# Performance work log

Measured on AMD Instinct MI355X. Metric: run time of the kernel, lower is better.

The kernel has to match this reference:

```python
import jax, jax.numpy as jnp
import numpy as np

V, T, E, H, L, B = 50257, 1024, 1024, 16, 12, 4
HD = E // H
FF = 4 * E
EPS = 1e-5


def layer_norm(x, g, b):
    m = jnp.mean(x, axis=-1, keepdims=True)
    v = jnp.mean((x - m) ** 2, axis=-1, keepdims=True)
    return (x - m) * jax.lax.rsqrt(v + EPS) * g + b


def setup_inputs() -> dict:
    key = jax.random.key(0)
    ks = jax.random.split(key, 24)
    s = 0.02
    inp = {
        'idx': jax.random.randint(ks[0], (B, T), 0, V),
        'targets': jax.random.randint(ks[1], (B, T), 0, V),
        'tok_emb': jax.random.normal(ks[2], (V, E), jnp.float32) * s,
        'pos_emb': jax.random.normal(ks[3], (T, E), jnp.float32) * s,
        'Wq': jax.random.normal(ks[4], (L, E, H, HD), jnp.float32) * s,
        'Wk': jax.random.normal(ks[5], (L, E, H, HD), jnp.float32) * s,
        'Wv': jax.random.normal(ks[6], (L, E, H, HD), jnp.float32) * s,
        'Wo': jax.random.normal(ks[7], (L, E, E), jnp.float32) * s,
        'bo': jnp.zeros((L, E), jnp.float32),
        'ln1_g': jnp.ones((L, E), jnp.float32),
        'ln1_b': jnp.zeros((L, E), jnp.float32),
        'ln2_g': jnp.ones((L, E), jnp.float32),
        'ln2_b': jnp.zeros((L, E), jnp.float32),
        'W1': jax.random.normal(ks[8], (L, E, FF), jnp.float32) * s,
        'b1': jnp.zeros((L, FF), jnp.float32),
        'W2': jax.random.normal(ks[9], (L, FF, E), jnp.float32) * s,
        'b2': jnp.zeros((L, E), jnp.float32),
        'lnf_g': jnp.ones((E,), jnp.float32),
        'lnf_b': jnp.zeros((E,), jnp.float32),
        'Whead': jax.random.normal(ks[10], (E, V), jnp.float32) * s,
        'bhead': jnp.zeros((V,), jnp.float32),
    }
    return inp


def forward(idx, targets, tok_emb, pos_emb, Wq, Wk, Wv, Wo, bo, ln1_g, ln1_b,
            ln2_g, ln2_b, W1, b1, W2, b2, lnf_g, lnf_b, Whead, bhead):
    Bc, Tc = idx.shape
    x = tok_emb[idx] + pos_emb[:Tc]  # [B,T,E]
    scale = HD ** -0.5
    causal = jnp.tril(jnp.ones((Tc, Tc), bool))
    for l in range(L):
        h = layer_norm(x, ln1_g[l], ln1_b[l])
        q = jnp.einsum('bte,ehd->bthd', h, Wq[l])
        k = jnp.einsum('bte,ehd->bthd', h, Wk[l])
        v = jnp.einsum('bte,ehd->bthd', h, Wv[l])
        wei = jnp.einsum('bqhd,bkhd->bhqk', q, k) * scale
        wei = jnp.where(causal, wei, -jnp.inf)
        wei = jax.nn.softmax(wei, axis=-1)
        att = jnp.einsum('bhqk,bkhd->bqhd', wei, v).reshape(Bc, Tc, E)
        x = x + att @ Wo[l] + bo[l]
        h = layer_norm(x, ln2_g[l], ln2_b[l])
        # torch nn.GELU default is exact (erf) gelu
        ff = jax.nn.gelu(h @ W1[l] + b1[l], approximate=False) @ W2[l] + b2[l]
        x = x + ff
    x = layer_norm(x, lnf_g, lnf_b)
    logits = x @ Whead + bhead  # [B,T,V]
    logp = jax.nn.log_softmax(logits, axis=-1)
    nll = -jnp.take_along_axis(logp, targets[..., None], axis=-1)[..., 0]
    loss = jnp.mean(nll)
    return logits, loss


def reference(idx, targets, tok_emb, pos_emb, Wq, Wk, Wv, Wo, bo, ln1_g, ln1_b,
              ln2_g, ln2_b, W1, b1, W2, b2, lnf_g, lnf_b, Whead, bhead):
    return forward(idx, targets, tok_emb, pos_emb, Wq, Wk, Wv, Wo, bo, ln1_g,
                   ln1_b, ln2_g, ln2_b, W1, b1, W2, b2, lnf_g, lnf_b, Whead, bhead)
```

## Files before the change

kernel.cpp:

```cpp
#include <hip/hip_runtime.h>
#include <cstdint>
#include <cstddef>

typedef unsigned short u16;
typedef __bf16 bf16x8 __attribute__((ext_vector_type(8)));
typedef float f32x4 __attribute__((ext_vector_type(4)));
typedef unsigned short u16x8 __attribute__((ext_vector_type(8)));
typedef unsigned short u16x4 __attribute__((ext_vector_type(4)));

constexpr int cV  = 50257;
constexpr int cVp = 50432;
constexpr int cNT = cVp / 256;
constexpr int cT  = 1024;
constexpr int cE  = 1024;
constexpr int cL  = 12;
constexpr int cFF = 4096;
constexpr int cBT = 4096;

__device__ __forceinline__ u16 f2bf(float f) {
  union { float f; unsigned u; } x; x.f = f;
  unsigned r = x.u + 0x7fffu + ((x.u >> 16) & 1u);
  return (u16)(r >> 16);
}

__device__ __forceinline__ void gload16(const void* g, void* l) {
  __builtin_amdgcn_global_load_lds(
      (const __attribute__((address_space(1))) void*)g,
      (__attribute__((address_space(3))) void*)l, 16, 0, 0);
}

__device__ __forceinline__ int swzoff(int row, int chunk) {
  return ((chunk ^ (row & 7) ^ ((row >> 3) & 7)) << 4);
}

__device__ __forceinline__ int xcd_swz(int id, int nwg) {
  if ((nwg & 7) == 0) { const int q = nwg >> 3; return (id & 7) * q + (id >> 3); }
  return id;
}

__global__ __launch_bounds__(256) void k_embed(const int* __restrict__ idx,
    const float* __restrict__ tok, const float* __restrict__ pos,
    float* __restrict__ x) {
  const int row = blockIdx.x;
  const int t = row & (cT - 1);
  const int tk = idx[row];
  const float4* tv = (const float4*)(tok + (size_t)tk * cE);
  const float4* pv = (const float4*)(pos + (size_t)t * cE);
  float4* xv = (float4*)(x + (size_t)row * cE);
  const int i = threadIdx.x;
  float4 a = tv[i];
  float4 p = pv[i];
  a.x += p.x; a.y += p.y; a.z += p.z; a.w += p.w;
  xv[i] = a;
}

__global__ __launch_bounds__(256) void k_ln(const float* __restrict__ x,
    const float* __restrict__ gw, const float* __restrict__ bw,
    u16* __restrict__ out) {
  const int row = blockIdx.x;
  const int t = threadIdx.x;
  const float4 v = ((const float4*)(x + (size_t)row * cE))[t];
  float s1 = v.x + v.y + v.z + v.w;
  float s2 = v.x * v.x + v.y * v.y + v.z * v.z + v.w * v.w;
  #pragma unroll
  for (int off = 32; off; off >>= 1) {
    s1 += __shfl_xor(s1, off);
    s2 += __shfl_xor(s2, off);
  }
  __shared__ float red[8];
  const int wid = t >> 6;
  if ((t & 63) == 0) { red[wid] = s1; red[4 + wid] = s2; }
  __syncthreads();
  s1 = red[0] + red[1] + red[2] + red[3];
  s2 = red[4] + red[5] + red[6] + red[7];
  const float mean = s1 * (1.0f / cE);
  const float var = s2 * (1.0f / cE) - mean * mean;
  const float rs = rsqrtf(var + 1e-5f);
  const float4 g4 = ((const float4*)gw)[t];
  const float4 b4 = ((const float4*)bw)[t];
  u16x4 o;
  o[0] = f2bf((v.x - mean) * rs * g4.x + b4.x);
  o[1] = f2bf((v.y - mean) * rs * g4.y + b4.y);
  o[2] = f2bf((v.z - mean) * rs * g4.z + b4.z);
  o[3] = f2bf((v.w - mean) * rs * g4.w + b4.w);
  *(u16x4*)(out + (size_t)row * cE + t * 4) = o;
}

__global__ __launch_bounds__(256) void k_cvt_t(const float* __restrict__ src,
    u16* __restrict__ dst, int K, int Nsrc, size_t sstride, size_t dstride) {
  __shared__ float tile[32][33];
  const float* s = src + blockIdx.z * sstride;
  u16* d = dst + blockIdx.z * dstride;
  const int n0 = blockIdx.x * 32, k0 = blockIdx.y * 32;
  const int t = threadIdx.x;
  const int c = t & 31, r0 = t >> 5;
  #pragma unroll
  for (int i = 0; i < 4; ++i) {
    const int kl = r0 + i * 8;
    const int n = n0 + c;
    tile[kl][c] = (n < Nsrc) ? s[(size_t)(k0 + kl) * Nsrc + n] : 0.0f;
  }
  __syncthreads();
  #pragma unroll
  for (int i = 0; i < 4; ++i) {
    const int nl = r0 + i * 8;
    d[(size_t)(n0 + nl) * K + k0 + c] = f2bf(tile[c][nl]);
  }
}

__device__ __forceinline__ void stage_half(const u16* __restrict__ Mb, int K,
    int kt, char* lds, int half, int tid) {
  #pragma unroll
  for (int p = 0; p < 2; ++p) {
    const int L = half * 1024 + p * 512 + tid;
    const int row = L >> 3, cc = L & 7;
    gload16(Mb + (size_t)row * K + kt + ((cc ^ (row & 7)) << 3),
            lds + (size_t)L * 16);
  }
}

template<int EPI>
__global__ __launch_bounds__(512) void k_gemm2(
    const u16* __restrict__ A, const u16* __restrict__ Bt,
    const float* __restrict__ bias, u16* __restrict__ obf,
    float* __restrict__ of, int K, int Nout, int ntile, int mt,
    float* __restrict__ pm, float* __restrict__ ps) {
  __shared__ __align__(16) char smem[131072];
  const int tid = threadIdx.x;
  const int lane = tid & 63;
  const int wid = tid >> 6;
  const int wg = xcd_swz((int)blockIdx.x, (int)gridDim.x);
  const int bm = wg % mt;
  const int bn = wg / mt;
  const int wm = wid >> 2, wn = wid & 3;
  const int l15 = lane & 15, lg = lane >> 4;

  f32x4 acc[8][4];
  #pragma unroll
  for (int i = 0; i < 8; ++i)
    #pragma unroll
    for (int j = 0; j < 4; ++j) { f32x4 z = {0.f,0.f,0.f,0.f}; acc[i][j] = z; }

  const u16* Ab = A + (size_t)(bm * 256) * K;
  const u16* Bb = Bt + (size_t)(bn * 256) * K;
  const int nt = K >> 6;

  {
    char* s0 = smem;
    char* s1 = smem + 65536;
    stage_half(Ab, K, 0, s0, 0, tid);
    stage_half(Bb, K, 0, s0 + 32768, 0, tid);
    stage_half(Bb, K, 0, s0 + 32768, 1, tid);
    stage_half(Ab, K, 0, s0, 1, tid);
    const int k1 = (nt > 1) ? 64 : 0;
    stage_half(Ab, K, k1, s1, 0, tid);
    stage_half(Bb, K, k1, s1 + 32768, 0, tid);
    stage_half(Bb, K, k1, s1 + 32768, 1, tid);
  }

  bf16x8 af[4][2], bfr[4][2];
  for (int t = 0; t < nt; ++t) {
    char* cs = smem + ((t & 1) << 16);
    char* co = smem + (((t & 1) ^ 1) << 16);
    const char* csB = cs + 32768;
    const int kn1 = (t + 1 < nt ? t + 1 : nt - 1) << 6;
    const int kn2 = (t + 2 < nt ? t + 2 : nt - 1) << 6;

    asm volatile("s_waitcnt vmcnt(6)" ::: "memory");
    __builtin_amdgcn_s_barrier();

    #pragma unroll
    for (int mi = 0; mi < 4; ++mi) {
      const int row = wm * 128 + mi * 16 + l15;
      #pragma unroll
      for (int kk = 0; kk < 2; ++kk)
        af[mi][kk] = *(const bf16x8*)(cs + row * 128 + (((kk * 4 + lg) ^ (row & 7)) << 4));
    }
    #pragma unroll
    for (int ni = 0; ni < 2; ++ni) {
      const int rowB = wn * 64 + ni * 16 + l15;
      #pragma unroll
      for (int kk = 0; kk < 2; ++kk)
        bfr[ni][kk] = *(const bf16x8*)(csB + rowB * 128 + (((kk * 4 + lg) ^ (rowB & 7)) << 4));
    }
    stage_half(Ab, K, kn1, co, 1, tid);
    __builtin_amdgcn_sched_barrier(0);
    __builtin_amdgcn_s_setprio(1);
    #pragma unroll
    for (int kk = 0; kk < 2; ++kk)
      #pragma unroll
      for (int ni = 0; ni < 2; ++ni)
        #pragma unroll
        for (int mi = 0; mi < 4; ++mi)
          acc[mi][ni] = __builtin_amdgcn_mfma_f32_16x16x32_bf16(af[mi][kk], bfr[ni][kk], acc[mi][ni], 0, 0, 0);
    __builtin_amdgcn_s_setprio(0);
    __builtin_amdgcn_sched_barrier(0);
    __builtin_amdgcn_s_barrier();

    #pragma unroll
    for (int ni = 2; ni < 4; ++ni) {
      const int rowB = wn * 64 + ni * 16 + l15;
      #pragma unroll
      for (int kk = 0; kk < 2; ++kk)
        bfr[ni][kk] = *(const bf16x8*)(csB + rowB * 128 + (((kk * 4 + lg) ^ (rowB & 7)) << 4));
    }
    __builtin_amdgcn_sched_barrier(0);
    __builtin_amdgcn_s_setprio(1);
    #pragma unroll
    for (int kk = 0; kk < 2; ++kk)
      #pragma unroll
      for (int ni = 2; ni < 4; ++ni)
        #pragma unroll
        for (int mi = 0; mi < 4; ++mi)
          acc[mi][ni] = __builtin_amdgcn_mfma_f32_16x16x32_bf16(af[mi][kk], bfr[ni][kk], acc[mi][ni], 0, 0, 0);
    __builtin_amdgcn_s_setprio(0);
    __builtin_amdgcn_sched_barrier(0);
    __builtin_amdgcn_s_barrier();

    #pragma unroll
    for (int mi = 0; mi < 4; ++mi) {
      const int row = wm * 128 + 64 + mi * 16 + l15;
      #pragma unroll
      for (int kk = 0; kk < 2; ++kk)
        af[mi][kk] = *(const bf16x8*)(cs + row * 128 + (((kk * 4 + lg) ^ (row & 7)) << 4));
    }
    stage_half(Ab, K, kn2, cs, 0, tid);
    stage_half(Bb, K, kn2, cs + 32768, 0, tid);
    stage_half(Bb, K, kn2, cs + 32768, 1, tid);
    __builtin_amdgcn_sched_barrier(0);
    __builtin_amdgcn_s_setprio(1);
    #pragma unroll
    for (int kk = 0; kk < 2; ++kk)
      #pragma unroll
      for (int ni = 0; ni < 2; ++ni)
        #pragma unroll
        for (int mi = 0; mi < 4; ++mi)
          acc[4 + mi][ni] = __builtin_amdgcn_mfma_f32_16x16x32_bf16(af[mi][kk], bfr[ni][kk], acc[4 + mi][ni], 0, 0, 0);
    __builtin_amdgcn_s_setprio(0);
    __builtin_amdgcn_sched_barrier(0);
    __builtin_amdgcn_s_barrier();

    __builtin_amdgcn_s_setprio(1);
    #pragma unroll
    for (int kk = 0; kk < 2; ++kk)
      #pragma unroll
      for (int ni = 2; ni < 4; ++ni)
        #pragma unroll
        for (int mi = 0; mi < 4; ++mi)
          acc[4 + mi][ni] = __builtin_amdgcn_mfma_f32_16x16x32_bf16(af[mi][kk], bfr[ni][kk], acc[4 + mi][ni], 0, 0, 0);
    __builtin_amdgcn_s_setprio(0);
    __builtin_amdgcn_sched_barrier(0);
  }
  asm volatile("s_waitcnt vmcnt(0)" ::: "memory");

  if constexpr (EPI == 3) {
    __syncthreads();
    float* pb = (float*)smem;
    #pragma unroll
    for (int m8 = 0; m8 < 8; ++m8) {
      const int grow = bm * 256 + wm * 128 + m8 * 16 + lg * 4;
      float rm[4];
      #pragma unroll
      for (int r = 0; r < 4; ++r) rm[r] = -1e30f;
      #pragma unroll
      for (int ni = 0; ni < 4; ++ni) {
        const int gcol = bn * 256 + wn * 64 + ni * 16 + l15;
        const bool ok = gcol < Nout;
        const float bb = ok ? bias[gcol] : 0.0f;
        #pragma unroll
        for (int r = 0; r < 4; ++r) {
          const float v = ok ? (acc[m8][ni][r] + bb) : -1e30f;
          acc[m8][ni][r] = v;
          if (ok) of[(size_t)(grow + r) * Nout + gcol] = v;
          rm[r] = fmaxf(rm[r], v);
        }
      }
      #pragma unroll
      for (int r = 0; r < 4; ++r) {
        float m = rm[r];
        #pragma unroll
        for (int off = 1; off < 16; off <<= 1) m = fmaxf(m, __shfl_xor(m, off));
        float s = 0.f;
        #pragma unroll
        for (int ni = 0; ni < 4; ++ni) s += __expf(acc[m8][ni][r] - m);
        #pragma unroll
        for (int off = 1; off < 16; off <<= 1) s += __shfl_xor(s, off);
        if (l15 == 0) {
          const int lrow = wm * 128 + m8 * 16 + lg * 4 + r;
          pb[(lrow * 4 + wn) * 2] = m;
          pb[(lrow * 4 + wn) * 2 + 1] = s;
        }
      }
    }
    __syncthreads();
    if (tid < 256) {
      float m = -1e30f, s = 0.f;
      #pragma unroll
      for (int q = 0; q < 4; ++q) {
        const float m2 = pb[(tid * 4 + q) * 2];
        const float s2 = pb[(tid * 4 + q) * 2 + 1];
        const float M = fmaxf(m, m2);
        s = s * __expf(m - M) + s2 * __expf(m2 - M);
        m = M;
      }
      const size_t grow = (size_t)(bm * 256 + tid);
      pm[grow * ntile + bn] = m;
      ps[grow * ntile + bn] = s;
    }
  } else {
    #pragma unroll
    for (int m8 = 0; m8 < 8; ++m8) {
      const int grow = bm * 256 + wm * 128 + m8 * 16 + lg * 4;
      #pragma unroll
      for (int ni = 0; ni < 4; ++ni) {
        const int gcol = bn * 256 + wn * 64 + ni * 16 + l15;
        #pragma unroll
        for (int r = 0; r < 4; ++r) {
          const float a = acc[m8][ni][r];
          if constexpr (EPI == 0) {
            obf[(size_t)(gcol >> 10) * 4194304 + (size_t)(grow + r) * 1024 + (gcol & 1023)] = f2bf(a);
          } else {
            const float gv = a + bias[gcol];
            obf[(size_t)(grow + r) * Nout + gcol] = f2bf(0.5f * gv * (1.0f + erff(gv * 0.70710678118f)));
          }
        }
      }
    }
  }
}

__global__ __launch_bounds__(256) void k_gemm_s(
    const u16* __restrict__ A, const u16* __restrict__ Bt,
    const float* __restrict__ bias, float* __restrict__ of,
    int K, int Nout, int mt) {
  __shared__ __align__(16) char smem[49152];
  const int tid = threadIdx.x;
  const int lane = tid & 63;
  const int wid = tid >> 6;
  const int wg = xcd_swz((int)blockIdx.x, (int)gridDim.x);
  const int bm = wg % mt;
  const int bn = wg / mt;
  const int wr = wid >> 1, wc = wid & 1;
  const int l15 = lane & 15, lg = lane >> 4;

  f32x4 acc[2][4];
  #pragma unroll
  for (int i = 0; i < 2; ++i)
    #pragma unroll
    for (int j = 0; j < 4; ++j) { f32x4 z = {0.f,0.f,0.f,0.f}; acc[i][j] = z; }

  const u16* Ab = A + (size_t)(bm * 64) * K;
  const u16* Bb = Bt + (size_t)(bn * 128) * K;
  const int nt = K >> 6;

  auto stage = [&](int t, char* buf) {
    const int kt = (t < nt ? t : nt - 1) << 6;
    #pragma unroll
    for (int p = 0; p < 2; ++p) {
      const int L = p * 256 + tid;
      const int row = L >> 3, cc = L & 7;
      gload16(Ab + (size_t)row * K + kt + ((cc ^ (row & 7)) << 3), buf + L * 16);
    }
    #pragma unroll
    for (int p = 0; p < 4; ++p) {
      const int L = p * 256 + tid;
      const int row = L >> 3, cc = L & 7;
      gload16(Bb + (size_t)row * K + kt + ((cc ^ (row & 7)) << 3), buf + 8192 + L * 16);
    }
  };
  stage(0, smem);
  stage(1, smem + 24576);

  for (int t = 0; t < nt; ++t) {
    char* cs = smem + ((t & 1) ? 24576 : 0);
    const char* csB = cs + 8192;
    asm volatile("s_waitcnt vmcnt(6)" ::: "memory");
    __builtin_amdgcn_s_barrier();

    bf16x8 af[2][2], bfr[4][2];
    #pragma unroll
    for (int mi = 0; mi < 2; ++mi) {
      const int row = wr * 32 + mi * 16 + l15;
      #pragma unroll
      for (int kk = 0; kk < 2; ++kk)
        af[mi][kk] = *(const bf16x8*)(cs + row * 128 + (((kk * 4 + lg) ^ (row & 7)) << 4));
    }
    #pragma unroll
    for (int ni = 0; ni < 4; ++ni) {
      const int row = wc * 64 + ni * 16 + l15;
      #pragma unroll
      for (int kk = 0; kk < 2; ++kk)
        bfr[ni][kk] = *(const bf16x8*)(csB + row * 128 + (((kk * 4 + lg) ^ (row & 7)) << 4));
    }
    __builtin_amdgcn_sched_barrier(0);
    __builtin_amdgcn_s_setprio(1);
    #pragma unroll
    for (int ni = 0; ni < 4; ++ni)
      #pragma unroll
      for (int mi = 0; mi < 2; ++mi)
        acc[mi][ni] = __builtin_amdgcn_mfma_f32_16x16x32_bf16(af[mi][0], bfr[ni][0], acc[mi][ni], 0, 0, 0);
    __builtin_amdgcn_s_setprio(0);
    __builtin_amdgcn_sched_barrier(0);
    asm volatile("s_waitcnt lgkmcnt(0)" ::: "memory");
    __builtin_amdgcn_sched_barrier(0);
    __builtin_amdgcn_s_barrier();

    stage(t + 2, cs);
    __builtin_amdgcn_sched_barrier(0);
    __builtin_amdgcn_s_setprio(1);
    #pragma unroll
    for (int ni = 0; ni < 4; ++ni)
      #pragma unroll
      for (int mi = 0; mi < 2; ++mi)
        acc[mi][ni] = __builtin_amdgcn_mfma_f32_16x16x32_bf16(af[mi][1], bfr[ni][1], acc[mi][ni], 0, 0, 0);
    __builtin_amdgcn_s_setprio(0);
    __builtin_amdgcn_sched_barrier(0);
  }
  asm volatile("s_waitcnt vmcnt(0)" ::: "memory");

  #pragma unroll
  for (int mi = 0; mi < 2; ++mi) {
    const int grow = bm * 64 + wr * 32 + mi * 16 + lg * 4;
    #pragma unroll
    for (int ni = 0; ni < 4; ++ni) {
      const int gcol = bn * 128 + wc * 64 + ni * 16 + l15;
      #pragma unroll
      for (int r = 0; r < 4; ++r)
        of[(size_t)(grow + r) * Nout + gcol] += acc[mi][ni][r] + bias[gcol];
    }
  }
}

__global__ __launch_bounds__(256) void k_gemm_legacy3(
    const u16* __restrict__ A, const float* __restrict__ B0,
    const float* __restrict__ bias, float* __restrict__ of,
    int M, int N, int K) {
  __shared__ u16 Al[128 * 32];
  __shared__ u16 Bl[32 * 128];
  const int tid = threadIdx.x;
  const int lane = tid & 63;
  const int wid = tid >> 6;
  const int bn = blockIdx.x;
  const int bm = blockIdx.y;
  const int wr = wid >> 1, wc = wid & 1;
  const int l15 = lane & 15, lg = lane >> 4;
  f32x4 acc[4][4];
  #pragma unroll
  for (int i = 0; i < 4; ++i)
    #pragma unroll
    for (int j = 0; j < 4; ++j) { f32x4 z = {0.f,0.f,0.f,0.f}; acc[i][j] = z; }
  const u16* Abase = A + (size_t)(bm * 128) * K;
  const int ar0 = tid >> 2;
  const int ac0 = (tid & 3) * 8;
  const int brow = tid >> 3;
  const int bc0 = (tid & 7) * 16;
  for (int kt = 0; kt < K; kt += 32) {
    *(u16x8*)(Al + ar0 * 32 + ac0) =
        *(const u16x8*)(Abase + (size_t)ar0 * K + kt + ac0);
    *(u16x8*)(Al + (ar0 + 64) * 32 + ac0) =
        *(const u16x8*)(Abase + (size_t)(ar0 + 64) * K + kt + ac0);
    {
      const float* bsrc = B0 + (size_t)(kt + brow) * N + bn * 128 + bc0;
      alignas(16) u16 tmp[16];
      const int colbase = bn * 128 + bc0;
      #pragma unroll
      for (int q = 0; q < 16; ++q)
        tmp[q] = f2bf((colbase + q < N) ? bsrc[q] : 0.0f);
      *(u16x8*)(Bl + brow * 128 + bc0) = *(const u16x8*)tmp;
      *(u16x8*)(Bl + brow * 128 + bc0 + 8) = *(const u16x8*)(tmp + 8);
    }
    __syncthreads();
    bf16x8 af[4];
    #pragma unroll
    for (int mi = 0; mi < 4; ++mi)
      af[mi] = *(const bf16x8*)(Al + (wr * 64 + mi * 16 + l15) * 32 + lg * 8);
    #pragma unroll
    for (int ni = 0; ni < 4; ++ni) {
      u16x8 tv;
      #pragma unroll
      for (int i = 0; i < 8; ++i)
        tv[i] = Bl[(lg * 8 + i) * 128 + wc * 64 + ni * 16 + l15];
      const bf16x8 bfr = __builtin_bit_cast(bf16x8, tv);
      #pragma unroll
      for (int mi = 0; mi < 4; ++mi)
        acc[mi][ni] = __builtin_amdgcn_mfma_f32_16x16x32_bf16(af[mi], bfr, acc[mi][ni], 0, 0, 0);
    }
    __syncthreads();
  }
  #pragma unroll
  for (int mi = 0; mi < 4; ++mi) {
    const int grow = bm * 128 + wr * 64 + mi * 16 + lg * 4;
    #pragma unroll
    for (int ni = 0; ni < 4; ++ni) {
      const int gcol = bn * 128 + wc * 64 + ni * 16 + l15;
      #pragma unroll
      for (int r = 0; r < 4; ++r)
        if (gcol < N) of[(size_t)(grow + r) * N + gcol] = acc[mi][ni][r] + bias[gcol];
    }
  }
}

__global__ __launch_bounds__(256, 2) void k_attn(
    const u16* __restrict__ qg, const u16* __restrict__ kg,
    const u16* __restrict__ vg, u16* __restrict__ og) {
  __shared__ u16 Kl[64 * 64];
  __shared__ u16 Vt[64 * 64];
  __shared__ u16 Pl[4][16 * 64];
  const int tid = threadIdx.x;
  const int lane = tid & 63;
  const int w = tid >> 6;
  const int qt = blockIdx.x;
  const int bh = blockIdx.y;
  const int b = bh >> 4, h = bh & 15;
  const int l15 = lane & 15, lg = lane >> 4;
  char* KlB = (char*)Kl;
  char* VtB = (char*)Vt;
  char* PlB = (char*)(Pl[w]);

  const size_t qrow0 = (size_t)b * cT + qt * 64 + w * 16;
  bf16x8 aq[2];
  #pragma unroll
  for (int c = 0; c < 2; ++c)
    aq[c] = *(const bf16x8*)(qg + (qrow0 + l15) * cE + h * 64 + c * 32 + lg * 8);

  f32x4 acco[4];
  #pragma unroll
  for (int j = 0; j < 4; ++j) { f32x4 z = {0.f,0.f,0.f,0.f}; acco[j] = z; }
  float mrun[4], lrun[4];
  #pragma unroll
  for (int r = 0; r < 4; ++r) { mrun[r] = -1e30f; lrun[r] = 0.f; }

  for (int kt = 0; kt <= qt; ++kt) {
    const size_t krow0 = (size_t)b * cT + kt * 64;
    #pragma unroll
    for (int u = 0; u < 2; ++u) {
      const int un = tid + u * 256;
      const int rr = un >> 3, c8 = (un & 7) * 8;
      *(u16x8*)(KlB + rr * 128 + swzoff(rr, c8 >> 3)) =
          *(const u16x8*)(kg + (krow0 + rr) * cE + h * 64 + c8);
      const u16x8 vv = *(const u16x8*)(vg + (krow0 + rr) * cE + h * 64 + c8);
      #pragma unroll
      for (int i = 0; i < 8; ++i)
        *(u16*)(VtB + (c8 + i) * 128 + swzoff(c8 + i, rr >> 3) + (rr & 7) * 2) = vv[i];
    }
    __syncthreads();

    f32x4 s[4];
    #pragma unroll
    for (int j = 0; j < 4; ++j) { f32x4 z = {0.f,0.f,0.f,0.f}; s[j] = z; }
    #pragma unroll
    for (int c = 0; c < 2; ++c) {
      #pragma unroll
      for (int j = 0; j < 4; ++j) {
        const int n = j * 16 + l15;
        const bf16x8 kb2 = *(const bf16x8*)(KlB + n * 128 + swzoff(n, c * 4 + lg));
        s[j] = __builtin_amdgcn_mfma_f32_16x16x32_bf16(aq[c], kb2, s[j], 0, 0, 0);
      }
    }

    float sv[4][4];
    const bool diag = (kt == qt);
    #pragma unroll
    for (int j = 0; j < 4; ++j)
      #pragma unroll
      for (int r = 0; r < 4; ++r) {
        float xs = s[j][r] * 0.125f;
        if (diag && (j * 16 + l15) > (w * 16 + lg * 4 + r)) xs = -1e30f;
        sv[j][r] = xs;
      }

    float corr[4];
    #pragma unroll
    for (int r = 0; r < 4; ++r) {
      float mx = fmaxf(fmaxf(sv[0][r], sv[1][r]), fmaxf(sv[2][r], sv[3][r]));
      #pragma unroll
      for (int off = 1; off < 16; off <<= 1) mx = fmaxf(mx, __shfl_xor(mx, off));
      const float mnew = fmaxf(mrun[r], mx);
      corr[r] = __expf(mrun[r] - mnew);
      float rs = 0.f;
      #pragma unroll
      for (int j = 0; j < 4; ++j) {
        const float p = __expf(sv[j][r] - mnew);
        sv[j][r] = p;
        rs += p;
      }
      #pragma unroll
      for (int off = 1; off < 16; off <<= 1) rs += __shfl_xor(rs, off);
      lrun[r] = lrun[r] * corr[r] + rs;
      mrun[r] = mnew;
    }

    #pragma unroll
    for (int j = 0; j < 4; ++j)
      #pragma unroll
      for (int r = 0; r < 4; ++r) {
        const int qr = lg * 4 + r, kc = j * 16 + l15;
        *(u16*)(PlB + qr * 128 + swzoff(qr, kc >> 3) + (kc & 7) * 2) = f2bf(sv[j][r]);
        acco[j][r] *= corr[r];
      }

    #pragma unroll
    for (int c = 0; c < 2; ++c) {
      const bf16x8 pa = *(const bf16x8*)(PlB + l15 * 128 + swzoff(l15, c * 4 + lg));
      #pragma unroll
      for (int j = 0; j < 4; ++j) {
        const int n = j * 16 + l15;
        const bf16x8 vb2 = *(const bf16x8*)(VtB + n * 128 + swzoff(n, c * 4 + lg));
        acco[j] = __builtin_amdgcn_mfma_f32_16x16x32_bf16(pa, vb2, acco[j], 0, 0, 0);
      }
    }
    __syncthreads();
  }

  #pragma unroll
  for (int j = 0; j < 4; ++j)
    #pragma unroll
    for (int r = 0; r < 4; ++r)
      og[(qrow0 + lg * 4 + r) * cE + h * 64 + j * 16 + l15] = f2bf(acco[j][r] / lrun[r]);
}

__global__ __launch_bounds__(256) void k_nll2(const float* __restrict__ pm,
    const float* __restrict__ ps, const float* __restrict__ logits,
    const int* __restrict__ tgt, float* __restrict__ nll, int NT) {
  const int row = blockIdx.x * 4 + (threadIdx.x >> 6);
  const int lane = threadIdx.x & 63;
  float m = -1e30f, s = 0.f;
  for (int i = lane; i < NT; i += 64) {
    const float m2 = pm[(size_t)row * NT + i];
    const float s2 = ps[(size_t)row * NT + i];
    const float M = fmaxf(m, m2);
    s = s * __expf(m - M) + s2 * __expf(m2 - M);
    m = M;
  }
  #pragma unroll
  for (int off = 1; off < 64; off <<= 1) {
    const float m2 = __shfl_xor(m, off);
    const float s2 = __shfl_xor(s, off);
    const float M = fmaxf(m, m2);
    s = s * __expf(m - M) + s2 * __expf(m2 - M);
    m = M;
  }
  if (lane == 0)
    nll[row] = logf(s) + m - logits[(size_t)row * cV + tgt[row]];
}

__global__ __launch_bounds__(256) void k_nll(const float* __restrict__ logits,
    const int* __restrict__ tgt, float* __restrict__ nll) {
  const int row = blockIdx.x;
  const float* lp = logits + (size_t)row * cV;
  const int t = threadIdx.x;
  __shared__ float red[8];
  const int wid = t >> 6, lane = t & 63;
  float mx = -1e30f;
  for (int i = t; i < cV; i += 256) mx = fmaxf(mx, lp[i]);
  #pragma unroll
  for (int off = 32; off; off >>= 1) mx = fmaxf(mx, __shfl_xor(mx, off));
  if (lane == 0) red[wid] = mx;
  __syncthreads();
  mx = fmaxf(fmaxf(red[0], red[1]), fmaxf(red[2], red[3]));
  float s = 0.f;
  for (int i = t; i < cV; i += 256) s += __expf(lp[i] - mx);
  #pragma unroll
  for (int off = 32; off; off >>= 1) s += __shfl_xor(s, off);
  if (lane == 0) red[4 + wid] = s;
  __syncthreads();
  if (t == 0) {
    s = red[4] + red[5] + red[6] + red[7];
    nll[row] = logf(s) + mx - lp[tgt[row]];
  }
}

__global__ __launch_bounds__(256) void k_loss(const float* __restrict__ nll,
    float* __restrict__ out) {
  const int t = threadIdx.x;
  float s = 0.f;
  for (int i = t; i < cBT; i += 256) s += nll[i];
  #pragma unroll
  for (int off = 32; off; off >>= 1) s += __shfl_xor(s, off);
  __shared__ float red[4];
  if ((t & 63) == 0) red[t >> 6] = s;
  __syncthreads();
  if (t == 0) out[0] = (red[0] + red[1] + red[2] + red[3]) * (1.0f / cBT);
}

extern "C" void kernel_launch(void* const* d_in, const int* in_sizes, int n_in,
                              void* d_out, int out_size, void* d_ws, size_t ws_size,
                              hipStream_t stream) {
  const int*   idx  = (const int*)d_in[0];
  const int*   tgt  = (const int*)d_in[1];
  const float* tok  = (const float*)d_in[2];
  const float* pos  = (const float*)d_in[3];
  const float* Wq   = (const float*)d_in[4];
  const float* Wk   = (const float*)d_in[5];
  const float* Wv   = (const float*)d_in[6];
  const float* Wo   = (const float*)d_in[7];
  const float* bo   = (const float*)d_in[8];
  const float* ln1g = (const float*)d_in[9];
  const float* ln1b = (const float*)d_in[10];
  const float* ln2g = (const float*)d_in[11];
  const float* ln2b = (const float*)d_in[12];
  const float* W1   = (const float*)d_in[13];
  const float* b1   = (const float*)d_in[14];
  const float* W2   = (const float*)d_in[15];
  const float* b2   = (const float*)d_in[16];
  const float* lnfg = (const float*)d_in[17];
  const float* lnfb = (const float*)d_in[18];
  const float* Wh   = (const float*)d_in[19];
  const float* bh   = (const float*)d_in[20];

  char* ob = (char*)d_out;
  float* x    = (float*)ob;
  u16* hb     = (u16*)(ob + (16u << 20));
  u16* qb     = (u16*)(ob + (24u << 20));
  u16* kb     = (u16*)(ob + (32u << 20));
  u16* vb     = (u16*)(ob + (40u << 20));
  u16* abuf   = (u16*)(ob + (48u << 20));
  u16* fbuf   = (u16*)(ob + (56u << 20));
  u16* W3T    = (u16*)(ob + (128u << 20));
  u16* WoT    = (u16*)(ob + (200u << 20));
  u16* W1T    = (u16*)(ob + (224u << 20));
  u16* W2T    = (u16*)(ob + (320u << 20));
  u16* hf     = (u16*)d_ws;
  float* nll  = (float*)((char*)d_ws + 8388608);
  u16* WheadT = (u16*)((char*)d_ws + 8404992);
  const size_t whead_end = 8404992u + (size_t)cVp * cE * 2u;
  float* pmax = (float*)((char*)d_ws + whead_end);
  float* psum = (float*)((char*)d_ws + whead_end + (size_t)cBT * cNT * 4);
  const size_t ws_need = whead_end + 2u * (size_t)cBT * cNT * 4;
  const bool fast_head = ws_size >= ws_need;

  float* logits = (float*)d_out;
  float* loss = logits + (size_t)cBT * cV;

  const dim3 blk(256);
  const size_t e2 = (size_t)cE * cE, ef = (size_t)cE * cFF;

  k_cvt_t<<<dim3(32, 32, cL), blk, 0, stream>>>(Wq, W3T,          cE, cE, e2, 3 * e2);
  k_cvt_t<<<dim3(32, 32, cL), blk, 0, stream>>>(Wk, W3T + e2,     cE, cE, e2, 3 * e2);
  k_cvt_t<<<dim3(32, 32, cL), blk, 0, stream>>>(Wv, W3T + 2 * e2, cE, cE, e2, 3 * e2);
  k_cvt_t<<<dim3(32, 32, cL), blk, 0, stream>>>(Wo, WoT, cE, cE, e2, e2);
  k_cvt_t<<<dim3(128, 32, cL), blk, 0, stream>>>(W1, W1T, cE, cFF, ef, ef);
  k_cvt_t<<<dim3(32, 128, cL), blk, 0, stream>>>(W2, W2T, cFF, cE, ef, ef);
  if (fast_head)
    k_cvt_t<<<dim3(cVp / 32, 32, 1), blk, 0, stream>>>(Wh, WheadT, cE, cV, 0, 0);

  k_embed<<<dim3(cBT), blk, 0, stream>>>(idx, tok, pos, x);
  for (int l = 0; l < cL; ++l) {
    k_ln<<<dim3(cBT), blk, 0, stream>>>(x, ln1g + l * cE, ln1b + l * cE, hb);
    k_gemm2<0><<<dim3(192), dim3(512), 0, stream>>>(hb, W3T + l * 3 * e2,
        nullptr, qb, nullptr, cE, 3072, 0, 16, nullptr, nullptr);
    k_attn<<<dim3(16, 64), blk, 0, stream>>>(qb, kb, vb, abuf);
    k_gemm_s<<<dim3(512), blk, 0, stream>>>(abuf, WoT + l * e2, bo + l * cE, x, cE, cE, 64);
    k_ln<<<dim3(cBT), blk, 0, stream>>>(x, ln2g + l * cE, ln2b + l * cE, hb);
    k_gemm2<2><<<dim3(256), dim3(512), 0, stream>>>(hb, W1T + l * ef,
        b1 + l * cFF, fbuf, nullptr, cE, cFF, 0, 16, nullptr, nullptr);
    k_gemm_s<<<dim3(512), blk, 0, stream>>>(fbuf, W2T + l * ef, b2 + l * cE, x, cFF, cE, 64);
  }
  k_ln<<<dim3(cBT), blk, 0, stream>>>(x, lnfg, lnfb, hf);
  if (fast_head) {
    k_gemm2<3><<<dim3(16 * cNT), dim3(512), 0, stream>>>(hf, WheadT, bh,
        nullptr, logits, cE, cV, cNT, 16, pmax, psum);
    k_nll2<<<dim3(cBT / 4), blk, 0, stream>>>(pmax, psum, logits, tgt, nll, cNT);
  } else {
    k_gemm_legacy3<<<dim3(393, 32), blk, 0, stream>>>(hf, Wh, bh, logits, cBT, cV, cE);
    k_nll<<<dim3(cBT), blk, 0, stream>>>(logits, tgt, nll);
  }
  k_loss<<<dim3(1), blk, 0, stream>>>(nll, loss);
}
```

Measured before the change: 4.663 ms.

## Shrink k_gemm2 tile to 128x256 with K=32 double buffer

Replaces the 256x256, K=64 triple-staged GEMM pipeline with a simpler 128x256 tile using K=32 steps and a plain two-buffer LDS scheme (48KB instead of 128KB), launch bounds set to allow more resident blocks, and XCD swizzle removed. Grids double so the small QKV/FF1 GEMMs fill more CUs. The cost is lower arithmetic intensity per tile, a full vmcnt(0) wait plus a barrier every iteration, and loss of the XCD-aware block ordering for L2 locality.

```diff
diff --git a/kernel.cpp b/kernel.cpp
--- a/kernel.cpp
+++ b/kernel.cpp
@@ -108,157 +108,87 @@
   }
 }
 
-__device__ __forceinline__ void stage_half(const u16* __restrict__ Mb, int K,
-    int kt, char* lds, int half, int tid) {
-  #pragma unroll
-  for (int p = 0; p < 2; ++p) {
-    const int L = half * 1024 + p * 512 + tid;
-    const int row = L >> 3, cc = L & 7;
-    gload16(Mb + (size_t)row * K + kt + ((cc ^ (row & 7)) << 3),
-            lds + (size_t)L * 16);
-  }
-}
-
 template<int EPI>
-__global__ __launch_bounds__(512) void k_gemm2(
+__global__ __launch_bounds__(512, 4) void k_gemm2(
     const u16* __restrict__ A, const u16* __restrict__ Bt,
     const float* __restrict__ bias, u16* __restrict__ obf,
     float* __restrict__ of, int K, int Nout, int ntile, int mt,
     float* __restrict__ pm, float* __restrict__ ps) {
-  __shared__ __align__(16) char smem[131072];
+  __shared__ __align__(16) char smem[49152];
   const int tid = threadIdx.x;
   const int lane = tid & 63;
   const int wid = tid >> 6;
-  const int wg = xcd_swz((int)blockIdx.x, (int)gridDim.x);
+  const int wg = (int)blockIdx.x;
   const int bm = wg % mt;
   const int bn = wg / mt;
   const int wm = wid >> 2, wn = wid & 3;
   const int l15 = lane & 15, lg = lane >> 4;
 
-  f32x4 acc[8][4];
-  #pragma unroll
-  for (int i = 0; i < 8; ++i)
+  f32x4 acc[4][4];
+  #pragma unroll
+  for (int i = 0; i < 4; ++i)
     #pragma unroll
     for (int j = 0; j < 4; ++j) { f32x4 z = {0.f,0.f,0.f,0.f}; acc[i][j] = z; }
 
-  const u16* Ab = A + (size_t)(bm * 256) * K;
+  const u16* Ab = A + (size_t)(bm * 128) * K;
   const u16* Bb = Bt + (size_t)(bn * 256) * K;
-  const int nt = K >> 6;
-
-  {
-    char* s0 = smem;
-    char* s1 = smem + 65536;
-    stage_half(Ab, K, 0, s0, 0, tid);
-    stage_half(Bb, K, 0, s0 + 32768, 0, tid);
-    stage_half(Bb, K, 0, s0 + 32768, 1, tid);
-    stage_half(Ab, K, 0, s0, 1, tid);
-    const int k1 = (nt > 1) ? 64 : 0;
-    stage_half(Ab, K, k1, s1, 0, tid);
-    stage_half(Bb, K, k1, s1 + 32768, 0, tid);
-    stage_half(Bb, K, k1, s1 + 32768, 1, tid);
-  }
-
-  bf16x8 af[4][2], bfr[4][2];
+  const int nt = K >> 5;
+
+  auto stage = [&](int t) {
+    char* buf = smem + ((t & 1) ? 24576 : 0);
+    const int kt = t << 5;
+    {
+      const int r = tid >> 2, c = tid & 3;
+      gload16(Ab + (size_t)r * K + kt + ((c ^ ((r >> 1) & 3)) << 3),
+              buf + tid * 16);
+    }
+    #pragma unroll
+    for (int p = 0; p < 2; ++p) {
+      const int L = p * 512 + tid;
+      const int r = L >> 2, c = L & 3;
+      gload16(Bb + (size_t)r * K + kt + ((c ^ ((r >> 1) & 3)) << 3),
+              buf + 8192 + L * 16);
+    }
+  };
+
+  stage(0);
+  asm volatile("s_waitcnt vmcnt(0)" ::: "memory");
+  __builtin_amdgcn_s_barrier();
+
   for (int t = 0; t < nt; ++t) {
-    char* cs = smem + ((t & 1) << 16);
-    char* co = smem + (((t & 1) ^ 1) << 16);
-    const char* csB = cs + 32768;
-    const int kn1 = (t + 1 < nt ? t + 1 : nt - 1) << 6;
-    const int kn2 = (t + 2 < nt ? t + 2 : nt - 1) << 6;
-
-    asm volatile("s_waitcnt vmcnt(6)" ::: "memory");
-    __builtin_amdgcn_s_barrier();
-
+    if (t + 1 < nt) stage(t + 1);
+    char* cs = smem + ((t & 1) ? 24576 : 0);
+    const char* csB = cs + 8192;
+    bf16x8 af[4], bfr[4];
     #pragma unroll
     for (int mi = 0; mi < 4; ++mi) {
-      const int row = wm * 128 + mi * 16 + l15;
-      #pragma unroll
-      for (int kk = 0; kk < 2; ++kk)
-        af[mi][kk] = *(const bf16x8*)(cs + row * 128 + (((kk * 4 + lg) ^ (row & 7)) << 4));
-    }
-    #pragma unroll
-    for (int ni = 0; ni < 2; ++ni) {
-      const int rowB = wn * 64 + ni * 16 + l15;
-      #pragma unroll
-      for (int kk = 0; kk < 2; ++kk)
-        bfr[ni][kk] = *(const bf16x8*)(csB + rowB * 128 + (((kk * 4 + lg) ^ (rowB & 7)) << 4));
-    }
-    stage_half(Ab, K, kn1, co, 1, tid);
+      const int row = wm * 64 + mi * 16 + l15;
+      af[mi] = *(const bf16x8*)(cs + row * 64 + ((lg ^ ((row >> 1) & 3)) << 4));
+    }
+    #pragma unroll
+    for (int ni = 0; ni < 4; ++ni) {
+      const int row = wn * 64 + ni * 16 + l15;
+      bfr[ni] = *(const bf16x8*)(csB + row * 64 + ((lg ^ ((row >> 1) & 3)) << 4));
+    }
     __builtin_amdgcn_sched_barrier(0);
     __builtin_amdgcn_s_setprio(1);
     #pragma unroll
-    for (int kk = 0; kk < 2; ++kk)
-      #pragma unroll
-      for (int ni = 0; ni < 2; ++ni)
-        #pragma unroll
-        for (int mi = 0; mi < 4; ++mi)
-          acc[mi][ni] = __builtin_amdgcn_mfma_f32_16x16x32_bf16(af[mi][kk], bfr[ni][kk], acc[mi][ni], 0, 0, 0);
+    for (int ni = 0; ni < 4; ++ni)
+      #pragma unroll
+      for (int mi = 0; mi < 4; ++mi)
+        acc[mi][ni] = __builtin_amdgcn_mfma_f32_16x16x32_bf16(af[mi], bfr[ni], acc[mi][ni], 0, 0, 0);
     __builtin_amdgcn_s_setprio(0);
     __builtin_amdgcn_sched_barrier(0);
+    asm volatile("s_waitcnt vmcnt(0)" ::: "memory");
     __builtin_amdgcn_s_barrier();
-
-    #pragma unroll
-    for (int ni = 2; ni < 4; ++ni) {
-      const int rowB = wn * 64 + ni * 16 + l15;
-      #pragma unroll
-      for (int kk = 0; kk < 2; ++kk)
-        bfr[ni][kk] = *(const bf16x8*)(csB + rowB * 128 + (((kk * 4 + lg) ^ (rowB & 7)) << 4));
-    }
-    __builtin_amdgcn_sched_barrier(0);
-    __builtin_amdgcn_s_setprio(1);
-    #pragma unroll
-    for (int kk = 0; kk < 2; ++kk)
-      #pragma unroll
-      for (int ni = 2; ni < 4; ++ni)
-        #pragma unroll
-        for (int mi = 0; mi < 4; ++mi)
-          acc[mi][ni] = __builtin_amdgcn_mfma_f32_16x16x32_bf16(af[mi][kk], bfr[ni][kk], acc[mi][ni], 0, 0, 0);
-    __builtin_amdgcn_s_setprio(0);
-    __builtin_amdgcn_sched_barrier(0);
-    __builtin_amdgcn_s_barrier();
-
-    #pragma unroll
-    for (int mi = 0; mi < 4; ++mi) {
-      const int row = wm * 128 + 64 + mi * 16 + l15;
-      #pragma unroll
-      for (int kk = 0; kk < 2; ++kk)
-        af[mi][kk] = *(const bf16x8*)(cs + row * 128 + (((kk * 4 + lg) ^ (row & 7)) << 4));
-    }
-    stage_half(Ab, K, kn2, cs, 0, tid);
-    stage_half(Bb, K, kn2, cs + 32768, 0, tid);
-    stage_half(Bb, K, kn2, cs + 32768, 1, tid);
-    __builtin_amdgcn_sched_barrier(0);
-    __builtin_amdgcn_s_setprio(1);
-    #pragma unroll
-    for (int kk = 0; kk < 2; ++kk)
-      #pragma unroll
-      for (int ni = 0; ni < 2; ++ni)
-        #pragma unroll
-        for (int mi = 0; mi < 4; ++mi)
-          acc[4 + mi][ni] = __builtin_amdgcn_mfma_f32_16x16x32_bf16(af[mi][kk], bfr[ni][kk], acc[4 + mi][ni], 0, 0, 0);
-    __builtin_amdgcn_s_setprio(0);
-    __builtin_amdgcn_sched_barrier(0);
-    __builtin_amdgcn_s_barrier();
-
-    __builtin_amdgcn_s_setprio(1);
-    #pragma unroll
-    for (int kk = 0; kk < 2; ++kk)
-      #pragma unroll
-      for (int ni = 2; ni < 4; ++ni)
-        #pragma unroll
-        for (int mi = 0; mi < 4; ++mi)
-          acc[4 + mi][ni] = __builtin_amdgcn_mfma_f32_16x16x32_bf16(af[mi][kk], bfr[ni][kk], acc[4 + mi][ni], 0, 0, 0);
-    __builtin_amdgcn_s_setprio(0);
-    __builtin_amdgcn_sched_barrier(0);
-  }
-  asm volatile("s_waitcnt vmcnt(0)" ::: "memory");
+  }
 
   if constexpr (EPI == 3) {
     __syncthreads();
     float* pb = (float*)smem;
     #pragma unroll
-    for (int m8 = 0; m8 < 8; ++m8) {
-      const int grow = bm * 256 + wm * 128 + m8 * 16 + lg * 4;
+    for (int mi = 0; mi < 4; ++mi) {
+      const int grow = bm * 128 + wm * 64 + mi * 16 + lg * 4;
       float rm[4];
       #pragma unroll
       for (int r = 0; r < 4; ++r) rm[r] = -1e30f;
@@ -269,8 +199,8 @@
         const float bb = ok ? bias[gcol] : 0.0f;
         #pragma unroll
         for (int r = 0; r < 4; ++r) {
-          const float v = ok ? (acc[m8][ni][r] + bb) : -1e30f;
-          acc[m8][ni][r] = v;
+          const float v = ok ? (acc[mi][ni][r] + bb) : -1e30f;
+          acc[mi][ni][r] = v;
           if (ok) of[(size_t)(grow + r) * Nout + gcol] = v;
           rm[r] = fmaxf(rm[r], v);
         }
@@ -282,18 +212,18 @@
         for (int off = 1; off < 16; off <<= 1) m = fmaxf(m, __shfl_xor(m, off));
         float s = 0.f;
         #pragma unroll
-        for (int ni = 0; ni < 4; ++ni) s += __expf(acc[m8][ni][r] - m);
+        for (int ni = 0; ni < 4; ++ni) s += __expf(acc[mi][ni][r] - m);
         #pragma unroll
         for (int off = 1; off < 16; off <<= 1) s += __shfl_xor(s, off);
         if (l15 == 0) {
-          const int lrow = wm * 128 + m8 * 16 + lg * 4 + r;
+          const int lrow = wm * 64 + mi * 16 + lg * 4 + r;
           pb[(lrow * 4 + wn) * 2] = m;
           pb[(lrow * 4 + wn) * 2 + 1] = s;
         }
       }
     }
     __syncthreads();
-    if (tid < 256) {
+    if (tid < 128) {
       float m = -1e30f, s = 0.f;
       #pragma unroll
       for (int q = 0; q < 4; ++q) {
@@ -303,20 +233,20 @@
         s = s * __expf(m - M) + s2 * __expf(m2 - M);
         m = M;
       }
-      const size_t grow = (size_t)(bm * 256 + tid);
+      const size_t grow = (size_t)(bm * 128 + tid);
       pm[grow * ntile + bn] = m;
       ps[grow * ntile + bn] = s;
     }
   } else {
     #pragma unroll
-    for (int m8 = 0; m8 < 8; ++m8) {
-      const int grow = bm * 256 + wm * 128 + m8 * 16 + lg * 4;
+    for (int mi = 0; mi < 4; ++mi) {
+      const int grow = bm * 128 + wm * 64 + mi * 16 + lg * 4;
       #pragma unroll
       for (int ni = 0; ni < 4; ++ni) {
         const int gcol = bn * 256 + wn * 64 + ni * 16 + l15;
         #pragma unroll
         for (int r = 0; r < 4; ++r) {
-          const float a = acc[m8][ni][r];
+          const float a = acc[mi][ni][r];
           if constexpr (EPI == 0) {
             obf[(size_t)(gcol >> 10) * 4194304 + (size_t)(grow + r) * 1024 + (gcol & 1023)] = f2bf(a);
           } else {
@@ -747,19 +677,19 @@
   k_embed<<<dim3(cBT), blk, 0, stream>>>(idx, tok, pos, x);
   for (int l = 0; l < cL; ++l) {
     k_ln<<<dim3(cBT), blk, 0, stream>>>(x, ln1g + l * cE, ln1b + l * cE, hb);
-    k_gemm2<0><<<dim3(192), dim3(512), 0, stream>>>(hb, W3T + l * 3 * e2,
-        nullptr, qb, nullptr, cE, 3072, 0, 16, nullptr, nullptr);
+    k_gemm2<0><<<dim3(32 * 12), dim3(512), 0, stream>>>(hb, W3T + l * 3 * e2,
+        nullptr, qb, nullptr, cE, 3072, 0, 32, nullptr, nullptr);
     k_attn<<<dim3(16, 64), blk, 0, stream>>>(qb, kb, vb, abuf);
     k_gemm_s<<<dim3(512), blk, 0, stream>>>(abuf, WoT + l * e2, bo + l * cE, x, cE, cE, 64);
     k_ln<<<dim3(cBT), blk, 0, stream>>>(x, ln2g + l * cE, ln2b + l * cE, hb);
-    k_gemm2<2><<<dim3(256), dim3(512), 0, stream>>>(hb, W1T + l * ef,
-        b1 + l * cFF, fbuf, nullptr, cE, cFF, 0, 16, nullptr, nullptr);
+    k_gemm2<2><<<dim3(32 * 16), dim3(512), 0, stream>>>(hb, W1T + l * ef,
+        b1 + l * cFF, fbuf, nullptr, cE, cFF, 0, 32, nullptr, nullptr);
     k_gemm_s<<<dim3(512), blk, 0, stream>>>(fbuf, W2T + l * ef, b2 + l * cE, x, cFF, cE, 64);
   }
   k_ln<<<dim3(cBT), blk, 0, stream>>>(x, lnfg, lnfb, hf);
   if (fast_head) {
-    k_gemm2<3><<<dim3(16 * cNT), dim3(512), 0, stream>>>(hf, WheadT, bh,
-        nullptr, logits, cE, cV, cNT, 16, pmax, psum);
+    k_gemm2<3><<<dim3(32 * cNT), dim3(512), 0, stream>>>(hf, WheadT, bh,
+        nullptr, logits, cE, cV, cNT, 32, pmax, psum);
     k_nll2<<<dim3(cBT / 4), blk, 0, stream>>>(pmax, psum, logits, tgt, nll, cNT);
   } else {
     k_gemm_legacy3<<<dim3(393, 32), blk, 0, stream>>>(hf, Wh, bh, logits, cBT, cV, cE);
```

Result: faster. 4.402 ms (-5.6%).
